# Performance work log

Measured on AMD Instinct MI355X. Metric: run time of the kernel, lower is better.

Reference implementation:

```python
import jax, jax.numpy as jnp
import numpy as np

# GeoTempScheduler default: init_temp=0.1, gamma=0.9, patience=1; at step 0 -> temp = 0.1
TEMP = 0.1

R, K, D, DLOW, B = 8, 10, 256, 10, 4096


def setup_inputs() -> dict:
    key = jax.random.key(0)
    k1, k2 = jax.random.split(key)
    x = jax.random.normal(k1, (B, D), dtype=jnp.float32)
    # reset_parameters: Us ~ N(0, 0.1/sqrt(D))
    Us = jax.random.normal(k2, (R, K, D, DLOW), dtype=jnp.float32) * (0.1 / np.sqrt(D))
    return {"x": x, "Us": Us}


def reference(x, Us):
    # encode: project data onto each (replicate, cluster) subspace basis
    # z: (r, k, B, d)
    z = jnp.einsum('bD,rkDd->rkbd', x, Us)
    # decode: x_ = z @ Us^T  -> (r, k, B, D)
    x_ = jnp.einsum('rkbd,rkDd->rkbD', z, Us)
    # l2-squared reconstruction loss, (r, k, B) -> permuted to (B, r, k)
    loss = 0.5 * jnp.sum((x_ - x) ** 2, axis=-1)
    assign_obj = jnp.transpose(loss, (2, 0, 1))  # (B, r, k)
    # set_assign uses detached objective (loss.data): temperature-scaled soft assignment
    c = jax.nn.softmax(-jax.lax.stop_gradient(assign_obj) / TEMP, axis=2)  # (B, r, k)
    # x_ * c.permute(1,2,0).unsqueeze(3), summed over clusters -> (r, B, D)
    out = jnp.einsum('rkbD,brk->rbD', x_, c)
    return out
```

## Files before the change

kernel.cpp:

```cpp
#include <hip/hip_runtime.h>
#include <math.h>

typedef unsigned short ushort_t;
typedef unsigned int uint32_tt;
typedef __attribute__((ext_vector_type(8))) short bf16x8;
typedef __attribute__((ext_vector_type(4))) float f32x4;

#define NR   8
#define NK   10
#define ND   256
#define NDL  10
#define NB   4096
#define NN   100
#define NP   128
#define NP2  128

#define WS_GP   0
#define WS_XB   32768
#define WS_U1   (32768 + 2097152)
#define WS_U2   (WS_U1 + 524288)
#define WS_NEED (WS_U2 + 524288)

#define L_US   0
#define L_ZB   34816
#define L_GP   60416
#define L_SIZE 64416

__device__ __forceinline__ ushort_t f2bf(float f) {
    uint32_tt u = __float_as_uint(f);
    u = (u + 0x7FFF + ((u >> 16) & 1)) >> 16;
    return (ushort_t)u;
}

__global__ __launch_bounds__(256) void prep_kernel(const float* __restrict__ x,
                                                   const float* __restrict__ Us,
                                                   char* __restrict__ ws) {
    __shared__ float lu[ND * NDL];
    const int bid = blockIdx.x, tid = threadIdx.x;

    if (bid >= 80) {
        ushort_t* xb = (ushort_t*)(ws + WS_XB);
        const int base = (bid - 80) * 1024;
        #pragma unroll
        for (int v = 0; v < 4; ++v) {
            int i = base + v * 256 + tid;
            float4 vv = ((const float4*)x)[i];
            uint32_tt p0 = (uint32_tt)f2bf(vv.x) | ((uint32_tt)f2bf(vv.y) << 16);
            uint32_tt p1 = (uint32_tt)f2bf(vv.z) | ((uint32_tt)f2bf(vv.w) << 16);
            ((uint2*)xb)[i] = make_uint2(p0, p1);
        }
        return;
    }

    const int rk = bid;
    const int r  = rk / NK, k = rk - r * NK;
    const float* U = Us + (size_t)rk * ND * NDL;
    for (int i = tid; i < 640; i += 256)
        ((float4*)lu)[i] = ((const float4*)U)[i];
    __syncthreads();

    float* Gp = (float*)(ws + WS_GP);
    if (tid < NDL * NDL) {
        int d1 = tid / NDL, d2 = tid - d1 * NDL;
        float acc = 0.f;
        #pragma unroll 8
        for (int Di = 0; Di < ND; ++Di)
            acc += lu[Di * NDL + d1] * lu[Di * NDL + d2];
        Gp[(size_t)rk * 100 + tid] = (d1 == d2 ? 10.0f : 0.0f) - 5.0f * acc;
    }

    ushort_t* u1 = (ushort_t*)(ws + WS_U1);
    for (int p = tid; p < ND * NDL; p += 256) {
        int d = p >> 8, D = p & 255;
        u1[((size_t)r * NP + k * NDL + d) * ND + D] = f2bf(lu[D * NDL + d]);
    }

    ushort_t* u2 = (ushort_t*)(ws + WS_U2);
    {
        int D = tid;
        uint32_tt* dst = (uint32_tt*)(u2 + ((size_t)r * ND + D) * NP2 + k * NDL);
        const float* src = lu + D * NDL;
        #pragma unroll
        for (int j = 0; j < 5; ++j)
            dst[j] = (uint32_tt)f2bf(src[2 * j]) | ((uint32_tt)f2bf(src[2 * j + 1]) << 16);
    }

    if (k == NK - 1) {
        for (int p = tid; p < 28 * ND; p += 256) {
            int n = p >> 8, D = p & 255;
            u1[((size_t)r * NP + 100 + n) * ND + D] = 0;
        }
        uint32_tt* u2u = (uint32_tt*)u2;
        #pragma unroll
        for (int j = 0; j < 14; ++j)
            u2u[((size_t)r * ND + tid) * (NP2 / 2) + 50 + j] = 0;
    }
}

__global__ __launch_bounds__(256, 2) void ksub_mfma11(const char* __restrict__ ws,
                                                      float* __restrict__ out) {
    __shared__ __align__(16) char smem[L_SIZE];
    char*  usb = smem + L_US;
    float* gp  = (float*)(smem + L_GP);

    const int tid  = threadIdx.x;
    const int w    = tid >> 6;
    const int lane = tid & 63;
    const int c    = lane & 15;
    const int q    = lane >> 4;
    const int bid  = blockIdx.x;
    const int r    = bid >> 6;
    const int bt   = bid & 63;
    const int b0   = bt * 64;
    const int wb   = w & 1;
    const int pair = w >> 1;
    const int bloc = wb * 16 + c;

    const ushort_t* xbp = (const ushort_t*)(ws + WS_XB) + (size_t)(b0 + bloc) * ND + q * 8;
    const ushort_t* u1b = (const ushort_t*)(ws + WS_U1) + (size_t)r * NP * ND;
    const ushort_t* u2b = (const ushort_t*)(ws + WS_U2) + (size_t)r * ND * NP2;
    const float*    gpg = (const float*)(ws + WS_GP) + (size_t)r * 1000;

    for (int i = tid; i < 1000; i += 256) gp[i] = gpg[i];

    bf16x8 sA[8], sB[8];

    const int sn0 = tid >> 4;
    const int sm  = tid & 15;

    #pragma unroll
    for (int j = 0; j < 8; ++j)
        sA[j] = *(const bf16x8*)(u1b + (size_t)(sn0 + j * 16) * ND + sm * 8);

    bf16x8 xf[2][4];
    #pragma unroll
    for (int tile = 0; tile < 2; ++tile)
        #pragma unroll
        for (int d = 0; d < 4; ++d)
            xf[tile][d] = *(const bf16x8*)(xbp + (size_t)tile * 32 * ND + d * 32);

    #pragma unroll
    for (int j = 0; j < 8; ++j)
        *(bf16x8*)(usb + (sn0 + j * 16) * 272 + sm * 16) = sA[j];
    __syncthreads();

    #pragma unroll
    for (int j = 0; j < 8; ++j)
        sB[j] = *(const bf16x8*)(u1b + 128 + (size_t)(sn0 + j * 16) * ND + sm * 8);

    f32x4 acc1[2][4];
    #pragma unroll
    for (int t2 = 0; t2 < 2; ++t2)
        #pragma unroll
        for (int tt = 0; tt < 4; ++tt) acc1[t2][tt] = (f32x4){0.f, 0.f, 0.f, 0.f};

    #pragma unroll
    for (int tt = 0; tt < 4; ++tt) {
        const int t = pair * 4 + tt;
        #pragma unroll
        for (int d = 0; d < 4; ++d) {
            bf16x8 uf = *(const bf16x8*)(usb + (t * 16 + c) * 272 + d * 64 + q * 16);
            acc1[0][tt] = __builtin_amdgcn_mfma_f32_16x16x32_bf16(uf, xf[0][d], acc1[0][tt], 0, 0, 0);
            acc1[1][tt] = __builtin_amdgcn_mfma_f32_16x16x32_bf16(uf, xf[1][d], acc1[1][tt], 0, 0, 0);
        }
    }
    __syncthreads();

    #pragma unroll
    for (int j = 0; j < 8; ++j)
        *(bf16x8*)(usb + (sn0 + j * 16) * 272 + sm * 16) = sB[j];
    #pragma unroll
    for (int tile = 0; tile < 2; ++tile)
        #pragma unroll
        for (int d = 0; d < 4; ++d)
            xf[tile][d] = *(const bf16x8*)(xbp + (size_t)tile * 32 * ND + (4 + d) * 32);
    __syncthreads();

    #pragma unroll
    for (int j = 0; j < 8; ++j)
        sA[j] = *(const bf16x8*)(u2b + (size_t)(sn0 + j * 16) * NP2 + sm * 8);

    #pragma unroll
    for (int tt = 0; tt < 4; ++tt) {
        const int t = pair * 4 + tt;
        #pragma unroll
        for (int d = 0; d < 4; ++d) {
            bf16x8 uf = *(const bf16x8*)(usb + (t * 16 + c) * 272 + d * 64 + q * 16);
            acc1[0][tt] = __builtin_amdgcn_mfma_f32_16x16x32_bf16(uf, xf[0][d], acc1[0][tt], 0, 0, 0);
            acc1[1][tt] = __builtin_amdgcn_mfma_f32_16x16x32_bf16(uf, xf[1][d], acc1[1][tt], 0, 0, 0);
        }
    }

    #pragma unroll
    for (int tile = 0; tile < 2; ++tile) {
        float* zb = (float*)(smem + L_ZB + tile * 12800);
        #pragma unroll
        for (int tt = 0; tt < 4; ++tt) {
            int t = pair * 4 + tt;
            #pragma unroll
            for (int rg = 0; rg < 4; ++rg) {
                int n = t * 16 + q * 4 + rg;
                if (n < NN) zb[bloc * 100 + n] = acc1[tile][tt][rg];
            }
        }
    }
    __syncthreads();

    #pragma unroll
    for (int j = 0; j < 8; ++j)
        *(bf16x8*)(usb + (sn0 + j * 16) * 272 + sm * 16) = sA[j];

    const int bsm = tid >> 3;
    const int kq  = tid & 7;
    #pragma unroll 1
    for (int tile = 0; tile < 2; ++tile) {
        float*    zb = (float*)(smem + L_ZB + tile * 12800);
        ushort_t* wt = (ushort_t*)(smem + L_ZB + tile * 8704);
        float zk[2][10], ee[2];
        {
            const float* zr = zb + bsm * 100;
            float L[2];
            #pragma unroll
            for (int jj = 0; jj < 2; ++jj) {
                int k = kq + 8 * jj;
                L[jj] = -1e30f;
                if (k < NK) {
                    #pragma unroll
                    for (int d = 0; d < 10; ++d) zk[jj][d] = zr[k * 10 + d];
                    const float* g = gp + k * 100;
                    float acc = 0.f;
                    #pragma unroll
                    for (int d1 = 0; d1 < 10; ++d1) {
                        float t2 = 0.f;
                        #pragma unroll
                        for (int d2 = 0; d2 < 10; ++d2) t2 += g[d1 * 10 + d2] * zk[jj][d2];
                        acc += t2 * zk[jj][d1];
                    }
                    L[jj] = acc;
                }
            }
            float m = fmaxf(L[0], L[1]);
            m = fmaxf(m, __shfl_xor(m, 1));
            m = fmaxf(m, __shfl_xor(m, 2));
            m = fmaxf(m, __shfl_xor(m, 4));
            float s = 0.f;
            #pragma unroll
            for (int jj = 0; jj < 2; ++jj) {
                ee[jj] = (kq + 8 * jj < NK) ? __expf(L[jj] - m) : 0.f;
                s += ee[jj];
            }
            s += __shfl_xor(s, 1);
            s += __shfl_xor(s, 2);
            s += __shfl_xor(s, 4);
            float inv = 1.0f / s;
            #pragma unroll
            for (int jj = 0; jj < 2; ++jj) ee[jj] *= inv;
        }
        __syncthreads();

        #pragma unroll
        for (int jj = 0; jj < 2; ++jj) {
            int k = kq + 8 * jj;
            if (k < NK) {
                #pragma unroll
                for (int d = 0; d < 10; ++d)
                    wt[bsm * 136 + k * 10 + d] = f2bf(ee[jj] * zk[jj][d]);
            }
        }
        {
            int row = tid >> 4, p = tid & 15;
            if (row < 32 && p < 14) ((uint32_tt*)wt)[row * 68 + 50 + p] = 0;
            row = (tid + 256) >> 4;
            if (row < 32 && p < 14) ((uint32_tt*)wt)[row * 68 + 50 + p] = 0;
        }
    }
    __syncthreads();

    const ushort_t* wt0 = (ushort_t*)(smem + L_ZB);
    const ushort_t* wt1 = (ushort_t*)(smem + L_ZB + 8704);
    const size_t orow = (size_t)r * NB + b0;

    #pragma unroll
    for (int j = 0; j < 8; ++j)
        sB[j] = *(const bf16x8*)(u2b + (size_t)(128 + sn0 + j * 16) * NP2 + sm * 8);

    {
        f32x4 acc3[2][4];
        #pragma unroll
        for (int t2 = 0; t2 < 2; ++t2)
            #pragma unroll
            for (int jj = 0; jj < 4; ++jj) acc3[t2][jj] = (f32x4){0.f, 0.f, 0.f, 0.f};

        #pragma unroll
        for (int nc = 0; nc < 4; ++nc) {
            bf16x8 bf0 = *(const bf16x8*)(wt0 + bloc * 136 + nc * 32 + q * 8);
            bf16x8 bf1 = *(const bf16x8*)(wt1 + bloc * 136 + nc * 32 + q * 8);
            #pragma unroll
            for (int jj = 0; jj < 4; ++jj) {
                bf16x8 af = *(const bf16x8*)(usb + (pair * 64 + jj * 16 + c) * 272 + nc * 64 + q * 16);
                acc3[0][jj] = __builtin_amdgcn_mfma_f32_16x16x32_bf16(af, bf0, acc3[0][jj], 0, 0, 0);
                acc3[1][jj] = __builtin_amdgcn_mfma_f32_16x16x32_bf16(af, bf1, acc3[1][jj], 0, 0, 0);
            }
        }
        #pragma unroll
        for (int tile = 0; tile < 2; ++tile)
            #pragma unroll
            for (int jj = 0; jj < 4; ++jj)
                __builtin_nontemporal_store(acc3[tile][jj],
                    (f32x4*)(out + (orow + tile * 32 + bloc) * ND + pair * 64 + jj * 16 + q * 4));
    }
    __syncthreads();

    #pragma unroll
    for (int j = 0; j < 8; ++j)
        *(bf16x8*)(usb + (sn0 + j * 16) * 272 + sm * 16) = sB[j];
    __syncthreads();

    {
        f32x4 acc3[2][4];
        #pragma unroll
        for (int t2 = 0; t2 < 2; ++t2)
            #pragma unroll
            for (int jj = 0; jj < 4; ++jj) acc3[t2][jj] = (f32x4){0.f, 0.f, 0.f, 0.f};

        #pragma unroll
        for (int nc = 0; nc < 4; ++nc) {
            bf16x8 bf0 = *(const bf16x8*)(wt0 + bloc * 136 + nc * 32 + q * 8);
            bf16x8 bf1 = *(const bf16x8*)(wt1 + bloc * 136 + nc * 32 + q * 8);
            #pragma unroll
            for (int jj = 0; jj < 4; ++jj) {
                bf16x8 af = *(const bf16x8*)(usb + (pair * 64 + jj * 16 + c) * 272 + nc * 64 + q * 16);
                acc3[0][jj] = __builtin_amdgcn_mfma_f32_16x16x32_bf16(af, bf0, acc3[0][jj], 0, 0, 0);
                acc3[1][jj] = __builtin_amdgcn_mfma_f32_16x16x32_bf16(af, bf1, acc3[1][jj], 0, 0, 0);
            }
        }
        #pragma unroll
        for (int tile = 0; tile < 2; ++tile)
            #pragma unroll
            for (int jj = 0; jj < 4; ++jj)
                __builtin_nontemporal_store(acc3[tile][jj],
                    (f32x4*)(out + (orow + tile * 32 + bloc) * ND + 128 + pair * 64 + jj * 16 + q * 4));
    }
}

#define XS_S 68
#define US_S 132
#define ZB_S 104
#define WT_S 68
#define U2_S 68
#define OFF_WT 0
#define OFF_SH 6800
#define OFF_GP 13600
#define SMEM_F 14600

__global__ __launch_bounds__(128) void gram_kernel(const float* __restrict__ Us,
                                                   float* __restrict__ Gp) {
    int rk = blockIdx.x;
    const float* U = Us + (size_t)rk * ND * NDL;
    __shared__ float u[ND * NDL];
    for (int i = threadIdx.x; i < ND * NDL; i += blockDim.x) u[i] = U[i];
    __syncthreads();
    int e = threadIdx.x;
    if (e < NDL * NDL) {
        int d1 = e / NDL, d2 = e % NDL;
        float acc = 0.f;
        #pragma unroll 8
        for (int Di = 0; Di < ND; ++Di)
            acc += u[Di * NDL + d1] * u[Di * NDL + d2];
        Gp[(size_t)rk * (NDL * NDL) + e] = (d1 == d2 ? 10.0f : 0.0f) - 5.0f * acc;
    }
}

__global__ __launch_bounds__(256, 2) void ksub_fused(const float* __restrict__ x,
                                                     const float* __restrict__ Us,
                                                     const float* __restrict__ Gp,
                                                     float* __restrict__ out) {
    __shared__ float smemf[SMEM_F];
    float* wT   = smemf + OFF_WT;
    float* xsf  = smemf + OFF_SH;
    float* usf  = smemf + OFF_SH + 2176;
    float* zbuf = smemf + OFF_SH;
    float* u2   = smemf + OFF_SH;
    float* gp   = smemf + OFF_GP;

    const int tid = threadIdx.x;
    const int r   = blockIdx.y;
    const int b0  = blockIdx.x * 64;

    for (int i = tid; i < NK * NDL * NDL; i += 256)
        gp[i] = Gp[(size_t)r * (NK * NDL * NDL) + i];

    const int nt = tid & 15;
    const int bt = tid >> 4;
    float acc[4][8];
    #pragma unroll
    for (int j = 0; j < 4; ++j)
        #pragma unroll
        for (int i = 0; i < 8; ++i) acc[j][i] = 0.f;

    for (int cch = 0; cch < 8; ++cch) {
        __syncthreads();
        for (int i = tid; i < 512; i += 256) {
            int b = i >> 3, f = i & 7;
            float4 v = ((const float4*)(x + (size_t)(b0 + b) * ND))[cch * 8 + f];
            float* dst = xsf + (f * 4) * XS_S + b;
            dst[0] = v.x; dst[XS_S] = v.y; dst[2 * XS_S] = v.z; dst[3 * XS_S] = v.w;
        }
        for (int p = tid; p < 320; p += 256) {
            int k = p >> 5, Dl = p & 31;
            const float* g = Us + ((size_t)((r * NK + k) * ND) + cch * 32 + Dl) * NDL;
            float* dst = usf + Dl * US_S + k * NDL;
            #pragma unroll
            for (int d = 0; d < 10; ++d) dst[d] = g[d];
        }
        __syncthreads();
        #pragma unroll 4
        for (int Dl = 0; Dl < 32; ++Dl) {
            float4 xv = *(const float4*)(xsf + Dl * XS_S + bt * 4);
            float4 ua = *(const float4*)(usf + Dl * US_S + nt * 8);
            float4 ub = *(const float4*)(usf + Dl * US_S + nt * 8 + 4);
            float xa[4] = {xv.x, xv.y, xv.z, xv.w};
            float uu[8] = {ua.x, ua.y, ua.z, ua.w, ub.x, ub.y, ub.z, ub.w};
            #pragma unroll
            for (int j = 0; j < 4; ++j)
                #pragma unroll
                for (int i = 0; i < 8; ++i) acc[j][i] += xa[j] * uu[i];
        }
    }
    __syncthreads();
    if (nt < 12) {
        #pragma unroll
        for (int j = 0; j < 4; ++j) {
            float* zp = zbuf + (bt * 4 + j) * ZB_S + nt * 8;
            *(float4*)(zp)     = make_float4(acc[j][0], acc[j][1], acc[j][2], acc[j][3]);
            *(float4*)(zp + 4) = make_float4(acc[j][4], acc[j][5], acc[j][6], acc[j][7]);
        }
    } else if (nt == 12) {
        #pragma unroll
        for (int j = 0; j < 4; ++j) {
            float* zp = zbuf + (bt * 4 + j) * ZB_S + 96;
            *(float4*)(zp) = make_float4(acc[j][0], acc[j][1], acc[j][2], acc[j][3]);
        }
    }
    __syncthreads();
    if (tid < 64) {
        const int b_l = tid;
        const float* zrow = zbuf + b_l * ZB_S;
        float L[10];
        #pragma unroll
        for (int k = 0; k < NK; ++k) {
            float zkk[10];
            #pragma unroll
            for (int d = 0; d < 10; ++d) zkk[d] = zrow[k * 10 + d];
            const float* g = gp + k * 100;
            float a2 = 0.f;
            #pragma unroll
            for (int d1 = 0; d1 < 10; ++d1) {
                float t = 0.f;
                #pragma unroll
                for (int d2 = 0; d2 < 10; ++d2) t += g[d1 * 10 + d2] * zkk[d2];
                a2 += t * zkk[d1];
            }
            L[k] = a2;
        }
        float m = L[0];
        #pragma unroll
        for (int k = 1; k < NK; ++k) m = fmaxf(m, L[k]);
        float e[10], s = 0.f;
        #pragma unroll
        for (int k = 0; k < NK; ++k) { e[k] = __expf(L[k] - m); s += e[k]; }
        float inv = 1.0f / s;
        #pragma unroll
        for (int k = 0; k < NK; ++k) {
            float ck = e[k] * inv;
            #pragma unroll
            for (int d = 0; d < 10; ++d)
                wT[(k * 10 + d) * WT_S + b_l] = ck * zrow[k * 10 + d];
        }
    }
    const int Dt  = tid & 15;
    const int bt2 = tid >> 4;
    for (int c2 = 0; c2 < 4; ++c2) {
        __syncthreads();
        for (int p = tid; p < 640; p += 256) {
            int k = p >> 6, Dl = p & 63;
            const float* g = Us + ((size_t)((r * NK + k) * ND) + c2 * 64 + Dl) * NDL;
            float* dst = u2 + (k * NDL) * U2_S + Dl;
            #pragma unroll
            for (int d = 0; d < 10; ++d) dst[d * U2_S] = g[d];
        }
        __syncthreads();
        float o[4][4];
        #pragma unroll
        for (int j = 0; j < 4; ++j)
            #pragma unroll
            for (int i = 0; i < 4; ++i) o[j][i] = 0.f;
        #pragma unroll 4
        for (int n = 0; n < NN; ++n) {
            float4 wv = *(const float4*)(wT + n * WT_S + bt2 * 4);
            float4 uv = *(const float4*)(u2 + n * U2_S + Dt * 4);
            float wa[4] = {wv.x, wv.y, wv.z, wv.w};
            float ub[4] = {uv.x, uv.y, uv.z, uv.w};
            #pragma unroll
            for (int j = 0; j < 4; ++j)
                #pragma unroll
                for (int i = 0; i < 4; ++i) o[j][i] += wa[j] * ub[i];
        }
        #pragma unroll
        for (int j = 0; j < 4; ++j) {
            float* op = out + ((size_t)r * NB + b0 + bt2 * 4 + j) * ND + c2 * 64 + Dt * 4;
            *(float4*)op = make_float4(o[j][0], o[j][1], o[j][2], o[j][3]);
        }
    }
}

extern "C" void kernel_launch(void* const* d_in, const int* in_sizes, int n_in,
                              void* d_out, int out_size, void* d_ws, size_t ws_size,
                              hipStream_t stream) {
    const float* x  = (const float*)d_in[0];
    const float* Us = (const float*)d_in[1];
    float* out = (float*)d_out;

    if (ws_size >= (size_t)WS_NEED) {
        prep_kernel<<<dim3(336), 256, 0, stream>>>(x, Us, (char*)d_ws);
        ksub_mfma11<<<dim3(512), 256, 0, stream>>>((const char*)d_ws, out);
    } else {
        gram_kernel<<<dim3(NR * NK), 128, 0, stream>>>(Us, (float*)d_ws);
        ksub_fused<<<dim3(NB / 64, NR), 256, 0, stream>>>(x, Us, (float*)d_ws, out);
    }
}
```

Measured before the change: 85.64 us.

## Fuse x bf16 conversion into main kernel and use LDS-only barriers

Drops the x-to-bf16 pass from the prep kernel, which shrinks its grid from 336 to 80 blocks. The main kernel now loads fp32 x directly and converts it to bf16 in registers, saving a 2MB workspace write and the matching read. It also replaces __syncthreads with a barrier that waits only on LDS counters, so outstanding global loads can stay in flight across barriers. The trade-off is twice the x bytes read per block, since x is replicated across 8 r-blocks, plus extra conversion ALU work. The weaker barrier is a correctness risk if any path relies on global memory ordering across it.

```diff
diff --git a/kernel.cpp b/kernel.cpp
--- a/kernel.cpp
+++ b/kernel.cpp
@@ -16,15 +16,20 @@
 #define NP2  128
 
 #define WS_GP   0
-#define WS_XB   32768
-#define WS_U1   (32768 + 2097152)
-#define WS_U2   (WS_U1 + 524288)
+#define WS_U1   32768
+#define WS_U2   (32768 + 524288)
 #define WS_NEED (WS_U2 + 524288)
 
 #define L_US   0
 #define L_ZB   34816
 #define L_GP   60416
 #define L_SIZE 64416
+
+#define LBAR() do { \
+    asm volatile("s_waitcnt lgkmcnt(0)" ::: "memory"); \
+    __builtin_amdgcn_s_barrier(); \
+    asm volatile("" ::: "memory"); \
+} while (0)
 
 __device__ __forceinline__ ushort_t f2bf(float f) {
     uint32_tt u = __float_as_uint(f);
@@ -32,25 +37,10 @@
     return (ushort_t)u;
 }
 
-__global__ __launch_bounds__(256) void prep_kernel(const float* __restrict__ x,
-                                                   const float* __restrict__ Us,
+__global__ __launch_bounds__(256) void prep_kernel(const float* __restrict__ Us,
                                                    char* __restrict__ ws) {
     __shared__ float lu[ND * NDL];
     const int bid = blockIdx.x, tid = threadIdx.x;
-
-    if (bid >= 80) {
-        ushort_t* xb = (ushort_t*)(ws + WS_XB);
-        const int base = (bid - 80) * 1024;
-        #pragma unroll
-        for (int v = 0; v < 4; ++v) {
-            int i = base + v * 256 + tid;
-            float4 vv = ((const float4*)x)[i];
-            uint32_tt p0 = (uint32_tt)f2bf(vv.x) | ((uint32_tt)f2bf(vv.y) << 16);
-            uint32_tt p1 = (uint32_tt)f2bf(vv.z) | ((uint32_tt)f2bf(vv.w) << 16);
-            ((uint2*)xb)[i] = make_uint2(p0, p1);
-        }
-        return;
-    }
 
     const int rk = bid;
     const int r  = rk / NK, k = rk - r * NK;
@@ -97,7 +87,8 @@
     }
 }
 
-__global__ __launch_bounds__(256, 2) void ksub_mfma11(const char* __restrict__ ws,
+__global__ __launch_bounds__(256, 2) void ksub_mfma12(const char* __restrict__ ws,
+                                                      const float* __restrict__ x,
                                                       float* __restrict__ out) {
     __shared__ __align__(16) char smem[L_SIZE];
     char*  usb = smem + L_US;
@@ -116,7 +107,7 @@
     const int pair = w >> 1;
     const int bloc = wb * 16 + c;
 
-    const ushort_t* xbp = (const ushort_t*)(ws + WS_XB) + (size_t)(b0 + bloc) * ND + q * 8;
+    const float*    xg  = x + (size_t)(b0 + bloc) * ND + q * 8;
     const ushort_t* u1b = (const ushort_t*)(ws + WS_U1) + (size_t)r * NP * ND;
     const ushort_t* u2b = (const ushort_t*)(ws + WS_U2) + (size_t)r * ND * NP2;
     const float*    gpg = (const float*)(ws + WS_GP) + (size_t)r * 1000;
@@ -124,7 +115,6 @@
     for (int i = tid; i < 1000; i += 256) gp[i] = gpg[i];
 
     bf16x8 sA[8], sB[8];
-
     const int sn0 = tid >> 4;
     const int sm  = tid & 15;
 
@@ -134,15 +124,25 @@
 
     bf16x8 xf[2][4];
     #pragma unroll
-    for (int tile = 0; tile < 2; ++tile)
-        #pragma unroll
-        for (int d = 0; d < 4; ++d)
-            xf[tile][d] = *(const bf16x8*)(xbp + (size_t)tile * 32 * ND + d * 32);
+    for (int tile = 0; tile < 2; ++tile) {
+        #pragma unroll
+        for (int d = 0; d < 4; ++d) {
+            const float* p = xg + (size_t)tile * 32 * ND + d * 32;
+            float4 a = *(const float4*)p;
+            float4 b = *(const float4*)(p + 4);
+            bf16x8 v;
+            v[0] = (short)f2bf(a.x); v[1] = (short)f2bf(a.y);
+            v[2] = (short)f2bf(a.z); v[3] = (short)f2bf(a.w);
+            v[4] = (short)f2bf(b.x); v[5] = (short)f2bf(b.y);
+            v[6] = (short)f2bf(b.z); v[7] = (short)f2bf(b.w);
+            xf[tile][d] = v;
+        }
+    }
 
     #pragma unroll
     for (int j = 0; j < 8; ++j)
         *(bf16x8*)(usb + (sn0 + j * 16) * 272 + sm * 16) = sA[j];
-    __syncthreads();
+    LBAR();
 
     #pragma unroll
     for (int j = 0; j < 8; ++j)
@@ -164,17 +164,27 @@
             acc1[1][tt] = __builtin_amdgcn_mfma_f32_16x16x32_bf16(uf, xf[1][d], acc1[1][tt], 0, 0, 0);
         }
     }
-    __syncthreads();
+    LBAR();
 
     #pragma unroll
     for (int j = 0; j < 8; ++j)
         *(bf16x8*)(usb + (sn0 + j * 16) * 272 + sm * 16) = sB[j];
     #pragma unroll
-    for (int tile = 0; tile < 2; ++tile)
-        #pragma unroll
-        for (int d = 0; d < 4; ++d)
-            xf[tile][d] = *(const bf16x8*)(xbp + (size_t)tile * 32 * ND + (4 + d) * 32);
-    __syncthreads();
+    for (int tile = 0; tile < 2; ++tile) {
+        #pragma unroll
+        for (int d = 0; d < 4; ++d) {
+            const float* p = xg + (size_t)tile * 32 * ND + (4 + d) * 32;
+            float4 a = *(const float4*)p;
+            float4 b = *(const float4*)(p + 4);
+            bf16x8 v;
+            v[0] = (short)f2bf(a.x); v[1] = (short)f2bf(a.y);
+            v[2] = (short)f2bf(a.z); v[3] = (short)f2bf(a.w);
+            v[4] = (short)f2bf(b.x); v[5] = (short)f2bf(b.y);
+            v[6] = (short)f2bf(b.z); v[7] = (short)f2bf(b.w);
+            xf[tile][d] = v;
+        }
+    }
+    LBAR();
 
     #pragma unroll
     for (int j = 0; j < 8; ++j)
@@ -204,7 +214,7 @@
             }
         }
     }
-    __syncthreads();
+    LBAR();
 
     #pragma unroll
     for (int j = 0; j < 8; ++j)
@@ -256,7 +266,7 @@
             #pragma unroll
             for (int jj = 0; jj < 2; ++jj) ee[jj] *= inv;
         }
-        __syncthreads();
+        LBAR();
 
         #pragma unroll
         for (int jj = 0; jj < 2; ++jj) {
@@ -274,7 +284,7 @@
             if (row < 32 && p < 14) ((uint32_tt*)wt)[row * 68 + 50 + p] = 0;
         }
     }
-    __syncthreads();
+    LBAR();
 
     const ushort_t* wt0 = (ushort_t*)(smem + L_ZB);
     const ushort_t* wt1 = (ushort_t*)(smem + L_ZB + 8704);
@@ -309,12 +319,12 @@
                 __builtin_nontemporal_store(acc3[tile][jj],
                     (f32x4*)(out + (orow + tile * 32 + bloc) * ND + pair * 64 + jj * 16 + q * 4));
     }
-    __syncthreads();
+    LBAR();
 
     #pragma unroll
     for (int j = 0; j < 8; ++j)
         *(bf16x8*)(usb + (sn0 + j * 16) * 272 + sm * 16) = sB[j];
-    __syncthreads();
+    LBAR();
 
     {
         f32x4 acc3[2][4];
@@ -522,8 +532,8 @@
     float* out = (float*)d_out;
 
     if (ws_size >= (size_t)WS_NEED) {
-        prep_kernel<<<dim3(336), 256, 0, stream>>>(x, Us, (char*)d_ws);
-        ksub_mfma11<<<dim3(512), 256, 0, stream>>>((const char*)d_ws, out);
+        prep_kernel<<<dim3(80), 256, 0, stream>>>(Us, (char*)d_ws);
+        ksub_mfma12<<<dim3(512), 256, 0, stream>>>((const char*)d_ws, x, out);
     } else {
         gram_kernel<<<dim3(NR * NK), 128, 0, stream>>>(Us, (float*)d_ws);
         ksub_fused<<<dim3(NB / 64, NR), 256, 0, stream>>>(x, Us, (float*)d_ws, out);
```

Result: slower. 88.50 us (+3.3%).
